# Optimization experiments

Measured on AMD Instinct MI355X. Metric: run time of the kernel, lower is better.

The kernel has to match this reference:

```python
import jax, jax.numpy as jnp
import numpy as np


def setup_inputs() -> dict:
    key = jax.random.key(0)
    ks = jax.random.split(key, 7)
    N, C, sy, sx = 1024, 384, 7, 7
    Dm, Dc = 64, 64
    Dg = C + Dm + Dc  # 512, must match f_t_global
    return {
        "f_t_global": jax.random.normal(ks[0], (N, Dg), dtype=jnp.float32),
        "x_t_local": jax.random.normal(ks[1], (N, C, sy, sx), dtype=jnp.float32),
        "x_t_prev_local": jax.random.normal(ks[2], (N, C, sy, sx), dtype=jnp.float32),
        "m_t": jax.random.normal(ks[3], (N, Dm), dtype=jnp.float32),
        "m_t_prev": jax.random.normal(ks[4], (N, Dm), dtype=jnp.float32),
        "c_t": jax.random.normal(ks[5], (N, Dc), dtype=jnp.float32),
        "c_t_prev": jax.random.normal(ks[6], (N, Dc), dtype=jnp.float32),
    }


def _join(loc, m, c):
    # loc: [S, N, C]; m: [N, Dm]; c: [N, Dc] -> [S, N, C+Dm+Dc]
    S, N, _ = loc.shape
    mc = jnp.concatenate([m, c], axis=-1)  # [N, Dm+Dc]
    mc = jnp.broadcast_to(mc[None], (S, N, mc.shape[-1]))
    return jnp.concatenate([loc, mc], axis=-1)


def _mean_ce_diag(logits):
    # logits: [S, N, N]; labels = arange(N) for every s -> mean over s of CE
    logp = jax.nn.log_softmax(logits, axis=-1)
    diag = jnp.diagonal(logp, axis1=1, axis2=2)  # [S, N]
    return -jnp.mean(diag)  # mean over N (per-step CE) and over S (the /(sx*sy))


def reference(f_t_global, x_t_local, x_t_prev_local, m_t, m_t_prev, c_t, c_t_prev):
    N, C, sy, sx = x_t_prev_local.shape
    S = sy * sx
    # [N,C,sy,sx] -> [S,N,C] (spatial locations batched)
    prev = x_t_prev_local.reshape(N, C, S).transpose(2, 0, 1)
    cur = x_t_local.reshape(N, C, S).transpose(2, 0, 1)
    pos = _join(prev, m_t_prev, c_t_prev)   # [S, N, D]
    # loss1: global features vs per-location previous positives
    logits1 = jnp.einsum('id,sjd->sij', f_t_global, pos)  # [S, N, N]
    loss1 = _mean_ce_diag(logits1)
    # loss2: per-location current predictions vs previous positives
    pred2 = _join(cur, m_t, c_t)            # [S, N, D]
    logits2 = jnp.einsum('sid,sjd->sij', pred2, pos)
    loss2 = _mean_ce_diag(logits2)
    loss = loss1 + loss2
    return (loss, x_t_prev_local, x_t_local)
```

## Files before the change

kernel.cpp:

```cpp
#include <hip/hip_runtime.h>
#include <hip/hip_bf16.h>

typedef __attribute__((ext_vector_type(8))) __bf16 bf16x8;
typedef __attribute__((ext_vector_type(4))) float  f32x4;

#define SDIM 49
#define NDIM 1024
#define CDIM 384
#define DDIM 512
#define DMC  64
#define SCALE (1.0f/(SDIM*NDIM))
#define SLOT 65536

__device__ __forceinline__ void gload16(const void* g, void* l) {
    __builtin_amdgcn_global_load_lds((const __attribute__((address_space(1))) void*)g,
                                     (__attribute__((address_space(3))) void*)l, 16, 0, 0);
}

__global__ __launch_bounds__(512) void pack_copy_kernel(
    const float* __restrict__ xloc, const float* __restrict__ mv,
    const float* __restrict__ cv,   __hip_bfloat16* __restrict__ dst,
    float* __restrict__ cpy)
{
    const int j = blockIdx.x;
    const int d = threadIdx.x;
    float vals[SDIM];
    if (d < CDIM) {
        const float* p = xloc + ((size_t)j * CDIM + d) * SDIM;
        #pragma unroll
        for (int s = 0; s < SDIM; ++s) vals[s] = p[s];
    } else if (d < CDIM + DMC) {
        float v = mv[j * DMC + (d - CDIM)];
        #pragma unroll
        for (int s = 0; s < SDIM; ++s) vals[s] = v;
    } else {
        float v = cv[j * DMC + (d - CDIM - DMC)];
        #pragma unroll
        for (int s = 0; s < SDIM; ++s) vals[s] = v;
    }
    #pragma unroll
    for (int s = 0; s < SDIM; ++s)
        dst[((size_t)s * NDIM + j) * DDIM + d] = __float2bfloat16(vals[s]);

    const float* src = xloc + (size_t)j * CDIM * SDIM;
    float* dcp = cpy + (size_t)j * CDIM * SDIM;
    for (int i = threadIdx.x; i < CDIM * SDIM; i += 512) dcp[i] = src[i];
}

__global__ void fpack_kernel(const float* __restrict__ f,
                             __hip_bfloat16* __restrict__ dst, int n)
{
    int i = blockIdx.x * blockDim.x + threadIdx.x;
    if (i < n) dst[i] = __float2bfloat16(f[i]);
}

__global__ __launch_bounds__(512, 2) void loss_kernel(
    const __hip_bfloat16* __restrict__ Fm,
    const __hip_bfloat16* __restrict__ Km,
    const __hip_bfloat16* __restrict__ Qm,
    float2* __restrict__ part,
    float* __restrict__ out)
{
    extern __shared__ __attribute__((aligned(16))) char sm[];

    const int bid = blockIdx.x;
    const int gid = (bid & 7) * 196 + (bid >> 3);
    const int s   = gid >> 5;
    const int rem = gid & 31;
    const int kb  = rem >> 3;
    const int qb  = rem & 7;

    const int tid  = threadIdx.x;
    const int lane = tid & 63;
    const int w    = tid >> 6;
    const int l15  = lane & 15;
    const int l4   = lane >> 4;
    const int wk   = w >> 2;
    const int wq   = w & 3;

    const char* Ag = (const char*)Km + ((size_t)s * NDIM + (size_t)kb * 256) * 1024;
    const char* Bg = (qb < 4)
        ? ((const char*)Fm + (size_t)qb * 256 * 1024)
        : ((const char*)Qm + ((size_t)s * NDIM + (size_t)(qb - 4) * 256) * 1024);

    const int trow = tid >> 3;
    const int scol = (((tid & 7) ^ ((tid >> 3) & 7)) << 4);

    #define STAGE_HALF(T, H) do {                                             \
        char* db_ = sm + (size_t)((T) & 1) * SLOT;                            \
        const size_t ko_ = (size_t)(T) * 128;                                 \
        _Pragma("unroll")                                                     \
        for (int c = 2 * (H); c < 2 * (H) + 2; ++c) {                         \
            gload16(Ag + (size_t)(c * 64 + trow) * 1024 + ko_ + scol,         \
                    db_ + c * 8192 + tid * 16);                               \
            gload16(Bg + (size_t)(c * 64 + trow) * 1024 + ko_ + scol,         \
                    db_ + 32768 + c * 8192 + tid * 16);                       \
        }                                                                     \
    } while (0)

    const unsigned xo   = (unsigned)((l15 & 7) << 4);
    const unsigned arow = (unsigned)((wk * 128 + l15) * 128);
    const unsigned brow = 32768u + (unsigned)((wq * 64 + l15) * 128);

    f32x4 acc[8][4];
    #pragma unroll
    for (int a = 0; a < 8; ++a)
        #pragma unroll
        for (int b = 0; b < 4; ++b) acc[a][b] = f32x4{0.f, 0.f, 0.f, 0.f};

    bf16x8 afr[4][2], bfr[4][2];

    #define READ_A(H) do {                                                    \
        _Pragma("unroll")                                                     \
        for (int a = 0; a < 4; ++a)                                           \
            _Pragma("unroll")                                                 \
            for (int kc = 0; kc < 2; ++kc)                                    \
                afr[a][kc] = *(const bf16x8*)(sb_ + arow + (H) * 8192u        \
                    + a * 2048u + (((unsigned)(kc * 64 + l4 * 16)) ^ xo));    \
    } while (0)

    #define READ_B(H) do {                                                    \
        _Pragma("unroll")                                                     \
        for (int b = 0; b < 2; ++b)                                           \
            _Pragma("unroll")                                                 \
            for (int kc = 0; kc < 2; ++kc)                                    \
                bfr[(H)*2 + b][kc] = *(const bf16x8*)(sb_ + brow              \
                    + ((H)*2 + b) * 2048u                                     \
                    + (((unsigned)(kc * 64 + l4 * 16)) ^ xo));                \
    } while (0)

    #define MFMA_Q(AH, BH) do {                                               \
        _Pragma("unroll")                                                     \
        for (int a = 0; a < 4; ++a)                                           \
            _Pragma("unroll")                                                 \
            for (int b = 0; b < 2; ++b)                                       \
                _Pragma("unroll")                                             \
                for (int kc = 0; kc < 2; ++kc)                                \
                    acc[(AH)*4 + a][(BH)*2 + b] =                             \
                        __builtin_amdgcn_mfma_f32_16x16x32_bf16(              \
                            afr[a][kc], bfr[(BH)*2 + b][kc],                  \
                            acc[(AH)*4 + a][(BH)*2 + b], 0, 0, 0);            \
    } while (0)

    STAGE_HALF(0, 0); STAGE_HALF(0, 1);
    asm volatile("s_waitcnt vmcnt(0)" ::: "memory");
    __builtin_amdgcn_s_barrier();

    for (int t = 0; t < 8; ++t) {
        const char* sb_ = sm + (size_t)(t & 1) * SLOT;
        const bool pf = (t < 7);
        READ_A(0); READ_B(0);
        if (pf) STAGE_HALF(t + 1, 0);
        __builtin_amdgcn_s_barrier();
        asm volatile("s_waitcnt lgkmcnt(0)" ::: "memory");
        __builtin_amdgcn_s_setprio(1); MFMA_Q(0, 0); __builtin_amdgcn_s_setprio(0);
        __builtin_amdgcn_s_barrier();
        READ_B(1);
        if (pf) STAGE_HALF(t + 1, 1);
        __builtin_amdgcn_s_barrier();
        asm volatile("s_waitcnt lgkmcnt(0)" ::: "memory");
        __builtin_amdgcn_s_setprio(1); MFMA_Q(0, 1); __builtin_amdgcn_s_setprio(0);
        __builtin_amdgcn_s_barrier();
        READ_A(1);
        __builtin_amdgcn_s_barrier();
        asm volatile("s_waitcnt lgkmcnt(0)" ::: "memory");
        __builtin_amdgcn_s_setprio(1); MFMA_Q(1, 0); __builtin_amdgcn_s_setprio(0);
        __builtin_amdgcn_s_barrier();
        asm volatile("s_waitcnt vmcnt(0)" ::: "memory");
        __builtin_amdgcn_s_barrier();
        __builtin_amdgcn_s_setprio(1); MFMA_Q(1, 1); __builtin_amdgcn_s_setprio(0);
        __builtin_amdgcn_s_barrier();
    }

    float q_m[4], q_s[4];
    #pragma unroll
    for (int b = 0; b < 4; ++b) {
        float m = -3.0e38f;
        #pragma unroll
        for (int a = 0; a < 8; ++a)
            #pragma unroll
            for (int r = 0; r < 4; ++r) m = fmaxf(m, acc[a][b][r]);
        float ss = 0.0f;
        #pragma unroll
        for (int a = 0; a < 8; ++a)
            #pragma unroll
            for (int r = 0; r < 4; ++r) ss += __expf(acc[a][b][r] - m);
        #pragma unroll
        for (int off = 16; off <= 32; off <<= 1) {
            float mo = __shfl_xor(m, off, 64);
            float so = __shfl_xor(ss, off, 64);
            float nm = fmaxf(m, mo);
            ss = ss * __expf(m - nm) + so * __expf(mo - nm);
            m = nm;
        }
        q_m[b] = m; q_s[b] = ss;
    }
    if (lane < 16) {
        const size_t rowb = (size_t)s * 2048 + (size_t)qb * 256 + wq * 64 + lane;
        #pragma unroll
        for (int b = 0; b < 4; ++b)
            part[(rowb + b * 16) * 8 + kb * 2 + wk] = make_float2(q_m[b], q_s[b]);
    }

    if (kb == (qb & 3) && (wq >> 1) == wk) {
        float d = 0.0f;
        const bool lok = (((lane >> 2) & 3) == l4);
        if (wq & 1) {
            #pragma unroll
            for (int b = 0; b < 4; ++b)
                #pragma unroll
                for (int r = 0; r < 4; ++r)
                    if (lok && r == (lane & 3)) d += acc[4 + b][b][r];
        } else {
            #pragma unroll
            for (int b = 0; b < 4; ++b)
                #pragma unroll
                for (int r = 0; r < 4; ++r)
                    if (lok && r == (lane & 3)) d += acc[b][b][r];
        }
        #pragma unroll
        for (int off = 1; off < 64; off <<= 1) d += __shfl_xor(d, off, 64);
        if (lane == 0) atomicAdd(out, -d * SCALE);
    }
    #undef STAGE_HALF
    #undef READ_A
    #undef READ_B
    #undef MFMA_Q
}

__global__ __launch_bounds__(256) void reduce_kernel(
    const float2* __restrict__ part, float* __restrict__ out)
{
    const int row = blockIdx.x * 256 + threadIdx.x;
    const float2* p = part + (size_t)row * 8;
    float m = -3.0e38f;
    float2 q[8];
    #pragma unroll
    for (int i = 0; i < 8; ++i) { q[i] = p[i]; m = fmaxf(m, q[i].x); }
    float ssum = 0.0f;
    #pragma unroll
    for (int i = 0; i < 8; ++i) ssum += q[i].y * __expf(q[i].x - m);
    float v = m + __logf(ssum);
    #pragma unroll
    for (int off = 1; off < 64; off <<= 1) v += __shfl_xor(v, off, 64);
    __shared__ float red[4];
    const int lane = threadIdx.x & 63, w = threadIdx.x >> 6;
    if (lane == 0) red[w] = v;
    __syncthreads();
    if (threadIdx.x == 0)
        atomicAdd(out, (red[0] + red[1] + red[2] + red[3]) * SCALE);
}

extern "C" void kernel_launch(void* const* d_in, const int* in_sizes, int n_in,
                              void* d_out, int out_size, void* d_ws, size_t ws_size,
                              hipStream_t stream)
{
    (void)in_sizes; (void)n_in; (void)out_size; (void)ws_size;
    const float* f  = (const float*)d_in[0];
    const float* x  = (const float*)d_in[1];
    const float* xp = (const float*)d_in[2];
    const float* mt = (const float*)d_in[3];
    const float* mp = (const float*)d_in[4];
    const float* ct = (const float*)d_in[5];
    const float* cp = (const float*)d_in[6];
    float* out = (float*)d_out;

    char* ws = (char*)d_ws;
    const size_t packBytes = (size_t)SDIM * NDIM * DDIM * 2;
    __hip_bfloat16* Km = (__hip_bfloat16*)ws;
    __hip_bfloat16* Qm = (__hip_bfloat16*)(ws + packBytes);
    __hip_bfloat16* Fm = (__hip_bfloat16*)(ws + 2 * packBytes);
    float2* part = (float2*)(ws + 2 * packBytes + (size_t)NDIM * DDIM * 2);

    hipMemsetAsync(out, 0, sizeof(float), stream);

    const int sz = NDIM * CDIM * SDIM;
    pack_copy_kernel<<<NDIM, 512, 0, stream>>>(xp, mp, cp, Km, out + 1);
    pack_copy_kernel<<<NDIM, 512, 0, stream>>>(x,  mt, ct, Qm, out + 1 + sz);
    fpack_kernel<<<(NDIM * DDIM + 255) / 256, 256, 0, stream>>>(f, Fm, NDIM * DDIM);

    loss_kernel<<<1568, 512, 2 * SLOT, stream>>>(Fm, Km, Qm, part, out);
    reduce_kernel<<<392, 256, 0, stream>>>(part, out);
}
```

Baseline: 252.5 us.

## Make loss kernel persistent with cross-tile prefetch; fuse input copy into pack

The loss GEMM kernel becomes persistent. It launches 256 blocks, and each block loops over its XCD's tile range with a stride of 32. The first K-chunk of the next tile is prefetched during the last step of the current tile, so the pipeline is not refilled from scratch for every tile. The per-step waits are restructured to match. Separately, the pack kernel now writes the passthrough copy of x from the values it has already loaded, instead of re-reading the input in a second loop. The persistent layout gives up some occupancy: 256 blocks of 512 threads may not fill every CU at two blocks per CU, and tiles are split unevenly across blocks (196/32), so there is a tail imbalance.

Result: slower. 260.0 us (+3.0%).

```diff
diff --git a/kernel.cpp b/kernel.cpp
--- a/kernel.cpp
+++ b/kernel.cpp
@@ -29,6 +29,9 @@
         const float* p = xloc + ((size_t)j * CDIM + d) * SDIM;
         #pragma unroll
         for (int s = 0; s < SDIM; ++s) vals[s] = p[s];
+        float* dcp = cpy + ((size_t)j * CDIM + d) * SDIM;
+        #pragma unroll
+        for (int s = 0; s < SDIM; ++s) dcp[s] = vals[s];
     } else if (d < CDIM + DMC) {
         float v = mv[j * DMC + (d - CDIM)];
         #pragma unroll
@@ -41,10 +44,6 @@
     #pragma unroll
     for (int s = 0; s < SDIM; ++s)
         dst[((size_t)s * NDIM + j) * DDIM + d] = __float2bfloat16(vals[s]);
-
-    const float* src = xloc + (size_t)j * CDIM * SDIM;
-    float* dcp = cpy + (size_t)j * CDIM * SDIM;
-    for (int i = threadIdx.x; i < CDIM * SDIM; i += 512) dcp[i] = src[i];
 }
 
 __global__ void fpack_kernel(const float* __restrict__ f,
@@ -64,11 +63,10 @@
     extern __shared__ __attribute__((aligned(16))) char sm[];
 
     const int bid = blockIdx.x;
-    const int gid = (bid & 7) * 196 + (bid >> 3);
-    const int s   = gid >> 5;
-    const int rem = gid & 31;
-    const int kb  = rem >> 3;
-    const int qb  = rem & 7;
+    const int xcd = bid & 7;
+    const int jj  = bid >> 3;
+    const int g0  = 196 * xcd;
+    const int gend = g0 + 196;
 
     const int tid  = threadIdx.x;
     const int lane = tid & 63;
@@ -78,36 +76,34 @@
     const int wk   = w >> 2;
     const int wq   = w & 3;
 
-    const char* Ag = (const char*)Km + ((size_t)s * NDIM + (size_t)kb * 256) * 1024;
-    const char* Bg = (qb < 4)
-        ? ((const char*)Fm + (size_t)qb * 256 * 1024)
-        : ((const char*)Qm + ((size_t)s * NDIM + (size_t)(qb - 4) * 256) * 1024);
-
     const int trow = tid >> 3;
     const int scol = (((tid & 7) ^ ((tid >> 3) & 7)) << 4);
-
-    #define STAGE_HALF(T, H) do {                                             \
-        char* db_ = sm + (size_t)((T) & 1) * SLOT;                            \
-        const size_t ko_ = (size_t)(T) * 128;                                 \
-        _Pragma("unroll")                                                     \
-        for (int c = 2 * (H); c < 2 * (H) + 2; ++c) {                         \
-            gload16(Ag + (size_t)(c * 64 + trow) * 1024 + ko_ + scol,         \
-                    db_ + c * 8192 + tid * 16);                               \
-            gload16(Bg + (size_t)(c * 64 + trow) * 1024 + ko_ + scol,         \
-                    db_ + 32768 + c * 8192 + tid * 16);                       \
-        }                                                                     \
-    } while (0)
 
     const unsigned xo   = (unsigned)((l15 & 7) << 4);
     const unsigned arow = (unsigned)((wk * 128 + l15) * 128);
     const unsigned brow = 32768u + (unsigned)((wq * 64 + l15) * 128);
 
+    auto APtr = [&](int gg) -> const char* {
+        const int s = gg >> 5, kb = (gg >> 3) & 3;
+        return (const char*)Km + ((size_t)s * NDIM + (size_t)kb * 256) * 1024;
+    };
+    auto BPtr = [&](int gg) -> const char* {
+        const int s = gg >> 5, qb = gg & 7;
+        return (qb < 4)
+            ? ((const char*)Fm + (size_t)qb * 256 * 1024)
+            : ((const char*)Qm + ((size_t)s * NDIM + (size_t)(qb - 4) * 256) * 1024);
+    };
+    auto stage4 = [&](const char* A, const char* B, int ko, char* slot, int h) {
+        #pragma unroll
+        for (int c = 2 * h; c < 2 * h + 2; ++c) {
+            gload16(A + (size_t)(c * 64 + trow) * 1024 + ko + scol,
+                    slot + c * 8192 + tid * 16);
+            gload16(B + (size_t)(c * 64 + trow) * 1024 + ko + scol,
+                    slot + 32768 + c * 8192 + tid * 16);
+        }
+    };
+
     f32x4 acc[8][4];
-    #pragma unroll
-    for (int a = 0; a < 8; ++a)
-        #pragma unroll
-        for (int b = 0; b < 4; ++b) acc[a][b] = f32x4{0.f, 0.f, 0.f, 0.f};
-
     bf16x8 afr[4][2], bfr[4][2];
 
     #define READ_A(H) do {                                                    \
@@ -142,87 +138,111 @@
                             acc[(AH)*4 + a][(BH)*2 + b], 0, 0, 0);            \
     } while (0)
 
-    STAGE_HALF(0, 0); STAGE_HALF(0, 1);
-    asm volatile("s_waitcnt vmcnt(0)" ::: "memory");
-    __builtin_amdgcn_s_barrier();
-
-    for (int t = 0; t < 8; ++t) {
-        const char* sb_ = sm + (size_t)(t & 1) * SLOT;
-        const bool pf = (t < 7);
-        READ_A(0); READ_B(0);
-        if (pf) STAGE_HALF(t + 1, 0);
-        __builtin_amdgcn_s_barrier();
-        asm volatile("s_waitcnt lgkmcnt(0)" ::: "memory");
-        __builtin_amdgcn_s_setprio(1); MFMA_Q(0, 0); __builtin_amdgcn_s_setprio(0);
-        __builtin_amdgcn_s_barrier();
-        READ_B(1);
-        if (pf) STAGE_HALF(t + 1, 1);
-        __builtin_amdgcn_s_barrier();
-        asm volatile("s_waitcnt lgkmcnt(0)" ::: "memory");
-        __builtin_amdgcn_s_setprio(1); MFMA_Q(0, 1); __builtin_amdgcn_s_setprio(0);
-        __builtin_amdgcn_s_barrier();
-        READ_A(1);
-        __builtin_amdgcn_s_barrier();
-        asm volatile("s_waitcnt lgkmcnt(0)" ::: "memory");
-        __builtin_amdgcn_s_setprio(1); MFMA_Q(1, 0); __builtin_amdgcn_s_setprio(0);
-        __builtin_amdgcn_s_barrier();
-        asm volatile("s_waitcnt vmcnt(0)" ::: "memory");
-        __builtin_amdgcn_s_barrier();
-        __builtin_amdgcn_s_setprio(1); MFMA_Q(1, 1); __builtin_amdgcn_s_setprio(0);
-        __builtin_amdgcn_s_barrier();
+    {
+        const char* A0 = APtr(g0 + jj);
+        const char* B0 = BPtr(g0 + jj);
+        stage4(A0, B0, 0, sm, 0);
+        stage4(A0, B0, 0, sm, 1);
     }
 
-    float q_m[4], q_s[4];
-    #pragma unroll
-    for (int b = 0; b < 4; ++b) {
-        float m = -3.0e38f;
+    for (int g = g0 + jj; g < gend; g += 32) {
+        const char* Ag = APtr(g);
+        const char* Bg = BPtr(g);
+        const bool hasNext = (g + 32) < gend;
+        const char* An = hasNext ? APtr(g + 32) : Ag;
+        const char* Bn = hasNext ? BPtr(g + 32) : Bg;
+
         #pragma unroll
         for (int a = 0; a < 8; ++a)
             #pragma unroll
-            for (int r = 0; r < 4; ++r) m = fmaxf(m, acc[a][b][r]);
-        float ss = 0.0f;
-        #pragma unroll
-        for (int a = 0; a < 8; ++a)
-            #pragma unroll
-            for (int r = 0; r < 4; ++r) ss += __expf(acc[a][b][r] - m);
-        #pragma unroll
-        for (int off = 16; off <= 32; off <<= 1) {
-            float mo = __shfl_xor(m, off, 64);
-            float so = __shfl_xor(ss, off, 64);
-            float nm = fmaxf(m, mo);
-            ss = ss * __expf(m - nm) + so * __expf(mo - nm);
-            m = nm;
-        }
-        q_m[b] = m; q_s[b] = ss;
+            for (int b = 0; b < 4; ++b) acc[a][b] = f32x4{0.f, 0.f, 0.f, 0.f};
+
+        #pragma unroll
+        for (int t = 0; t < 8; ++t) {
+            const char* sb_ = sm + (size_t)(t & 1) * SLOT;
+            char* ns_ = sm + (size_t)((t + 1) & 1) * SLOT;
+            const bool pf = (t < 7) || hasNext;
+            const char* sA = (t < 7) ? Ag : An;
+            const char* sB = (t < 7) ? Bg : Bn;
+            const int ko = (t < 7) ? (t + 1) * 128 : 0;
+
+            asm volatile("s_waitcnt vmcnt(0)" ::: "memory");
+            __builtin_amdgcn_s_barrier();
+            if (pf) stage4(sA, sB, ko, ns_, 0);
+            READ_A(0); READ_B(0);
+            __builtin_amdgcn_s_barrier();
+            asm volatile("s_waitcnt lgkmcnt(0)" ::: "memory");
+            __builtin_amdgcn_s_setprio(1); MFMA_Q(0, 0); __builtin_amdgcn_s_setprio(0);
+            __builtin_amdgcn_s_barrier();
+            if (pf) stage4(sA, sB, ko, ns_, 1);
+            READ_B(1);
+            __builtin_amdgcn_s_barrier();
+            asm volatile("s_waitcnt lgkmcnt(0)" ::: "memory");
+            __builtin_amdgcn_s_setprio(1); MFMA_Q(0, 1); __builtin_amdgcn_s_setprio(0);
+            __builtin_amdgcn_s_barrier();
+            READ_A(1);
+            __builtin_amdgcn_s_barrier();
+            asm volatile("s_waitcnt lgkmcnt(0)" ::: "memory");
+            __builtin_amdgcn_s_setprio(1); MFMA_Q(1, 0); __builtin_amdgcn_s_setprio(0);
+            __builtin_amdgcn_s_barrier();
+            __builtin_amdgcn_s_setprio(1); MFMA_Q(1, 1); __builtin_amdgcn_s_setprio(0);
+        }
+
+        const int s  = g >> 5;
+        const int kb = (g >> 3) & 3;
+        const int qb = g & 7;
+
+        float q_m[4], q_s[4];
+        #pragma unroll
+        for (int b = 0; b < 4; ++b) {
+            float m = -3.0e38f;
+            #pragma unroll
+            for (int a = 0; a < 8; ++a)
+                #pragma unroll
+                for (int r = 0; r < 4; ++r) m = fmaxf(m, acc[a][b][r]);
+            float ss = 0.0f;
+            #pragma unroll
+            for (int a = 0; a < 8; ++a)
+                #pragma unroll
+                for (int r = 0; r < 4; ++r) ss += __expf(acc[a][b][r] - m);
+            #pragma unroll
+            for (int off = 16; off <= 32; off <<= 1) {
+                float mo = __shfl_xor(m, off, 64);
+                float so = __shfl_xor(ss, off, 64);
+                float nm = fmaxf(m, mo);
+                ss = ss * __expf(m - nm) + so * __expf(mo - nm);
+                m = nm;
+            }
+            q_m[b] = m; q_s[b] = ss;
+        }
+        if (lane < 16) {
+            const size_t rowb = (size_t)s * 2048 + (size_t)qb * 256 + wq * 64 + lane;
+            #pragma unroll
+            for (int b = 0; b < 4; ++b)
+                part[(rowb + b * 16) * 8 + kb * 2 + wk] = make_float2(q_m[b], q_s[b]);
+        }
+
+        if (kb == (qb & 3) && (wq >> 1) == wk) {
+            float d = 0.0f;
+            const bool lok = (((lane >> 2) & 3) == l4);
+            if (wq & 1) {
+                #pragma unroll
+                for (int b = 0; b < 4; ++b)
+                    #pragma unroll
+                    for (int r = 0; r < 4; ++r)
+                        if (lok && r == (lane & 3)) d += acc[4 + b][b][r];
+            } else {
+                #pragma unroll
+                for (int b = 0; b < 4; ++b)
+                    #pragma unroll
+                    for (int r = 0; r < 4; ++r)
+                        if (lok && r == (lane & 3)) d += acc[b][b][r];
+            }
+            #pragma unroll
+            for (int off = 1; off < 64; off <<= 1) d += __shfl_xor(d, off, 64);
+            if (lane == 0) atomicAdd(out, -d * SCALE);
+        }
     }
-    if (lane < 16) {
-        const size_t rowb = (size_t)s * 2048 + (size_t)qb * 256 + wq * 64 + lane;
-        #pragma unroll
-        for (int b = 0; b < 4; ++b)
-            part[(rowb + b * 16) * 8 + kb * 2 + wk] = make_float2(q_m[b], q_s[b]);
-    }
-
-    if (kb == (qb & 3) && (wq >> 1) == wk) {
-        float d = 0.0f;
-        const bool lok = (((lane >> 2) & 3) == l4);
-        if (wq & 1) {
-            #pragma unroll
-            for (int b = 0; b < 4; ++b)
-                #pragma unroll
-                for (int r = 0; r < 4; ++r)
-                    if (lok && r == (lane & 3)) d += acc[4 + b][b][r];
-        } else {
-            #pragma unroll
-            for (int b = 0; b < 4; ++b)
-                #pragma unroll
-                for (int r = 0; r < 4; ++r)
-                    if (lok && r == (lane & 3)) d += acc[b][b][r];
-        }
-        #pragma unroll
-        for (int off = 1; off < 64; off <<= 1) d += __shfl_xor(d, off, 64);
-        if (lane == 0) atomicAdd(out, -d * SCALE);
-    }
-    #undef STAGE_HALF
     #undef READ_A
     #undef READ_B
     #undef MFMA_Q
@@ -279,6 +299,6 @@
     pack_copy_kernel<<<NDIM, 512, 0, stream>>>(x,  mt, ct, Qm, out + 1 + sz);
     fpack_kernel<<<(NDIM * DDIM + 255) / 256, 256, 0, stream>>>(f, Fm, NDIM * DDIM);
 
-    loss_kernel<<<1568, 512, 2 * SLOT, stream>>>(Fm, Km, Qm, part, out);
+    loss_kernel<<<256, 512, 2 * SLOT, stream>>>(Fm, Km, Qm, part, out);
     reduce_kernel<<<392, 256, 0, stream>>>(part, out);
 }
```
